# Optimization experiments

Hardware: AMD Instinct MI355X
Metric: run time of the kernel (lower is better)

Reference implementation:

```python
import jax, jax.numpy as jnp
import numpy as np

B, L, D, R, NTYPES, NLAYERS = 8, 96, 512, 64, 47, 3
BN_EPS = 1e-3  # keras BatchNormalization default epsilon


def setup_inputs() -> dict:
    key = jax.random.key(0)
    ks = jax.random.split(key, 12)
    text = jax.random.normal(ks[0], (B, L, D), dtype=jnp.float32)
    # binary token mask; force first token on so counts are never zero
    input_mask = (jax.random.uniform(ks[1], (B, L)) < 0.8).astype(jnp.float32)
    input_mask = input_mask.at[:, 0].set(1.0)
    dep_adj = (jax.random.uniform(ks[2], (B, L, L)) < 0.1).astype(jnp.float32)
    dep_value = jax.random.randint(ks[3], (B, L, L), 0, NTYPES, dtype=jnp.int32)
    dep_emb_table = jax.random.normal(ks[4], (NTYPES, D), dtype=jnp.float32) * 0.05
    bn_gamma = jnp.ones((D,), jnp.float32)
    bn_beta = jnp.zeros((D,), jnp.float32)
    W_stack = jax.random.normal(ks[5], (NLAYERS, D, D), dtype=jnp.float32) * 0.02
    b_stack = jax.random.normal(ks[6], (NLAYERS, D), dtype=jnp.float32) * 0.02
    ensemble_linear = jnp.ones((NLAYERS,), jnp.float32)
    fc_W = jax.random.normal(ks[7], (D, R), dtype=jnp.float32) * 0.02
    fc_b = jnp.zeros((R,), jnp.float32)
    return {"text": text, "input_mask": input_mask, "dep_adj": dep_adj,
            "dep_emb_table": dep_emb_table, "bn_gamma": bn_gamma, "bn_beta": bn_beta,
            "W_stack": W_stack, "b_stack": b_stack, "ensemble_linear": ensemble_linear,
            "fc_W": fc_W, "fc_b": fc_b, "dep_value": dep_value}


def _masked_avg(mask, x):
    # get_average: sum over masked tokens / count of nonzero mask entries
    m = mask[:, :, None]                       # [B,L,1]
    x_sum = jnp.sum(x * m, axis=1)             # [B,D]
    cnt = jnp.sum((m != 0).astype(x.dtype), axis=1)  # [B,1]
    return x_sum / (cnt + 1e-10)


def reference(text, input_mask, dep_adj, dep_emb_table, bn_gamma, bn_beta,
              W_stack, b_stack, ensemble_linear, fc_W, fc_b, dep_value):
    # dep embedding + switch_layer: zero out rows where dep type id == 0
    dep_embed = dep_emb_table[dep_value]                           # [B,L,L,D]
    dep_embed = dep_embed * (dep_value > 0)[..., None].astype(dep_embed.dtype)

    # BatchNormalization at inference (moving mean 0, var 1) + identity dropout
    seq = text * (bn_gamma / jnp.sqrt(1.0 + BN_EPS)) + bn_beta     # [B,L,D]

    scale = 1.0 / np.float32(np.power(D, 0.5))
    pools = []
    for l in range(NLAYERS):
        # get_attention: sum_k cat(x_i, e_ij)_k * cat(x_j, e_ji)_k
        #              = x_i . x_j + e_ij . e_ji
        score = (jnp.einsum('bid,bjd->bij', seq, seq)
                 + jnp.einsum('bijd,bjid->bij', dep_embed, dep_embed)) * scale
        attn = jax.nn.softmax(score, axis=-1) * dep_adj            # [B,L,L]
        # TypeGraphConvolution: out_i = sum_j attn_ij * ((x_j + e_ji) @ W) + b
        # (W applied after the attn-weighted aggregation; same linear math)
        agg = (jnp.einsum('bij,bjd->bid', attn, seq)
               + jnp.einsum('bij,bjid->bid', attn, dep_embed))      # [B,L,D]
        seq = jax.nn.relu(agg @ W_stack[l] + b_stack[l])
        pools.append(_masked_avg(input_mask, seq))

    x_pool = jnp.stack(pools, axis=-1)                              # [B,D,3]
    ens = jnp.sum(x_pool * jax.nn.softmax(ensemble_linear), axis=-1)  # [B,D]
    return ens @ fc_W + fc_b                                        # [B,R]
```

## Files before the change

### kernel.cpp

```cpp
#include <hip/hip_runtime.h>
#include <math.h>

#define SCALE 0.044194173824159216f
#define INVS  0.9995003746879289f

#define SEQ_OFF  0
#define AGG_OFF  393216
#define G_OFF    786432
#define POOL_OFF 788736
#define ENSW_OFF 801024
#define CNT_OFF  801028

#define F4FMA(acc, s, ww) { acc.x = fmaf(s, ww.x, acc.x); acc.y = fmaf(s, ww.y, acc.y); \
                            acc.z = fmaf(s, ww.z, acc.z); acc.w = fmaf(s, ww.w, acc.w); }

__device__ __forceinline__ float wave_sum(float v) {
  #pragma unroll
  for (int o = 32; o; o >>= 1) v += __shfl_xor(v, o);
  return v;
}
__device__ __forceinline__ float wave_max(float v) {
  #pragma unroll
  for (int o = 32; o; o >>= 1) v = fmaxf(v, __shfl_xor(v, o));
  return v;
}

__global__ __launch_bounds__(256) void k_prep(
    const float* __restrict__ text, const float* __restrict__ mask,
    const float* __restrict__ E, const float* __restrict__ gamma,
    const float* __restrict__ beta, const float* __restrict__ ensl,
    float* __restrict__ ws)
{
  const int blk = blockIdx.x, tid = threadIdx.x;
  const int gt = blk * 256 + tid;
  {
    const float4* T4 = (const float4*)text;
    float4* S4 = (float4*)(ws + SEQ_OFF);
    const float4* G4 = (const float4*)gamma;
    const float4* B4 = (const float4*)beta;
    for (int i4 = gt; i4 < 98304; i4 += 512 * 256) {
      float4 t = T4[i4];
      const int gi = i4 & 127;
      const float4 g4 = G4[gi], b4 = B4[gi];
      float4 o;
      o.x = fmaf(t.x, g4.x * INVS, b4.x);
      o.y = fmaf(t.y, g4.y * INVS, b4.y);
      o.z = fmaf(t.z, g4.z * INVS, b4.z);
      o.w = fmaf(t.w, g4.w * INVS, b4.w);
      S4[i4] = o;
    }
  }
  const int wg = gt >> 6, lane = tid & 63;
  float* G = ws + G_OFF;
  for (int g = wg; g < 2209; g += 2048) {
    const int t1 = g / 47, t2 = g - t1 * 47;
    const float4* e1 = (const float4*)E + t1 * 128;
    const float4* e2 = (const float4*)E + t2 * 128;
    const float4 a0 = e1[lane * 2], a1 = e1[lane * 2 + 1];
    const float4 b0 = e2[lane * 2], b1 = e2[lane * 2 + 1];
    float d = a0.x * b0.x;
    d = fmaf(a0.y, b0.y, d); d = fmaf(a0.z, b0.z, d); d = fmaf(a0.w, b0.w, d);
    d = fmaf(a1.x, b1.x, d); d = fmaf(a1.y, b1.y, d);
    d = fmaf(a1.z, b1.z, d); d = fmaf(a1.w, b1.w, d);
    d = wave_sum(d);
    if (lane == 0) G[g] = d;
  }
  if (blk == 0) {
    if (tid < 8) {
      float c = 0.f;
      for (int i = 0; i < 96; ++i) c += (mask[tid * 96 + i] != 0.f) ? 1.f : 0.f;
      (ws + CNT_OFF)[tid] = 1.f / (c + 1e-10f);
    }
    if (tid == 8) {
      const float e0 = ensl[0], e1 = ensl[1], e2 = ensl[2];
      const float m = fmaxf(e0, fmaxf(e1, e2));
      const float x0 = expf(e0 - m), x1 = expf(e1 - m), x2 = expf(e2 - m);
      const float s = x0 + x1 + x2;
      (ws + ENSW_OFF)[0] = x0 / s;
      (ws + ENSW_OFF)[1] = x1 / s;
      (ws + ENSW_OFF)[2] = x2 / s;
    }
  }
}

__device__ __forceinline__ void pool_unit(int u, int tid,
    const float* __restrict__ seq, const float* __restrict__ mask,
    const float* __restrict__ rcnt, float* __restrict__ dst)
{
  const int b = u >> 1;
  const int d = (u & 1) * 256 + tid;
  float acc = 0.f;
  #pragma unroll 4
  for (int i = 0; i < 96; ++i)
    acc = fmaf(mask[b * 96 + i], seq[(b * 96 + i) * 512 + d], acc);
  dst[b * 512 + d] = acc * rcnt[b];
}

__global__ __launch_bounds__(256) void k_attn(
    const float* __restrict__ seq, float* __restrict__ agg,
    const float* __restrict__ adj, const float* __restrict__ E,
    const int* __restrict__ dv, const float* __restrict__ ws,
    const float* __restrict__ mask, float* __restrict__ pool_dst, int do_pool)
{
  const int blk = blockIdx.x, tid = threadIdx.x;
  if (blk >= 768) {
    if (do_pool) pool_unit(blk - 768, tid, seq, mask, ws + CNT_OFF, pool_dst);
    return;
  }
  __shared__ float s_sc[96];
  __shared__ float s_at[96];
  __shared__ int   s_vt[96];
  const int b = blk & 7, i = blk >> 3;
  const int w = tid >> 6, lane = tid & 63;
  const float* G = ws + G_OFF;
  const float4* seq4 = (const float4*)seq + (size_t)b * 96 * 128;

  const float4 q0 = seq4[i * 128 + lane * 2];
  const float4 q1 = seq4[i * 128 + lane * 2 + 1];
  #pragma unroll 2
  for (int j = w; j < 96; j += 4) {
    const float4 x0 = seq4[j * 128 + lane * 2];
    const float4 x1 = seq4[j * 128 + lane * 2 + 1];
    float d = q0.x * x0.x;
    d = fmaf(q0.y, x0.y, d); d = fmaf(q0.z, x0.z, d); d = fmaf(q0.w, x0.w, d);
    d = fmaf(q1.x, x1.x, d); d = fmaf(q1.y, x1.y, d);
    d = fmaf(q1.z, x1.z, d); d = fmaf(q1.w, x1.w, d);
    d = wave_sum(d);
    if (lane == 0) s_sc[j] = d;
  }
  __syncthreads();
  const int* dvb = dv + b * 9216;
  if (tid < 96) {
    const int v1 = dvb[i * 96 + tid];
    const int v2 = dvb[tid * 96 + i];
    s_vt[tid] = v2;
    const float bs = (v1 > 0 && v2 > 0) ? G[v1 * 47 + v2] : 0.f;
    s_sc[tid] = (s_sc[tid] + bs) * SCALE;
  }
  __syncthreads();
  if (w == 0) {
    const float v0 = s_sc[lane];
    const float v1 = (lane < 32) ? s_sc[64 + lane] : -3.0e38f;
    const float mx = wave_max(fmaxf(v0, v1));
    const float e0 = expf(v0 - mx);
    const float e1 = (lane < 32) ? expf(v1 - mx) : 0.f;
    const float s = wave_sum(e0 + e1);
    const float inv = 1.f / s;
    const float* ad = adj + (b * 96 + i) * 96;
    s_at[lane] = e0 * inv * ad[lane];
    if (lane < 32) s_at[64 + lane] = e1 * inv * ad[64 + lane];
  }
  __syncthreads();
  const int d2 = w * 64 + lane;
  const float2* seq2 = (const float2*)seq + (size_t)b * 96 * 256;
  const float2* E2 = (const float2*)E;
  float ax = 0.f, ay = 0.f;
  for (int j = 0; j < 96; ++j) {
    const float a = s_at[j];
    if (a != 0.f) {
      float2 x = seq2[j * 256 + d2];
      const int vt = s_vt[j];
      if (vt > 0) {
        const float2 e2v = E2[vt * 256 + d2];
        x.x += e2v.x; x.y += e2v.y;
      }
      ax = fmaf(a, x.x, ax);
      ay = fmaf(a, x.y, ay);
    }
  }
  float2 o; o.x = ax; o.y = ay;
  ((float2*)agg)[(size_t)(b * 96 + i) * 256 + d2] = o;
}

__global__ __launch_bounds__(256) void k_gemm(
    const float* __restrict__ A, const float* __restrict__ W,
    const float* __restrict__ bias, float* __restrict__ Out)
{
  __shared__ __align__(16) float s_a[6 * 512];
  __shared__ __align__(16) float4 s_p[8 * 6 * 32];
  const int blk = blockIdx.x, tid = threadIdx.x;
  const int b = blk & 7, rr = (blk >> 3) & 15, ct = blk >> 7;
  const int rt = b * 16 + rr;
  const int r0 = rt * 6, c0 = ct * 128;
  {
    const float4* A4 = (const float4*)(A + r0 * 512);
    float4* sa4 = (float4*)s_a;
    sa4[tid] = A4[tid];
    sa4[tid + 256] = A4[tid + 256];
    sa4[tid + 512] = A4[tid + 512];
  }
  __syncthreads();
  const int cq = tid & 31, kq = tid >> 5;
  const float4* W4 = (const float4*)W + ct * 32 + cq;
  float4 acc[6];
  #pragma unroll
  for (int r = 0; r < 6; ++r) { acc[r].x = 0.f; acc[r].y = 0.f; acc[r].z = 0.f; acc[r].w = 0.f; }
  const float4* sa4 = (const float4*)s_a;
  #pragma unroll 2
  for (int k4 = kq * 16; k4 < kq * 16 + 16; ++k4) {
    const float4 w0 = W4[(k4 * 4 + 0) * 128];
    const float4 w1 = W4[(k4 * 4 + 1) * 128];
    const float4 w2 = W4[(k4 * 4 + 2) * 128];
    const float4 w3 = W4[(k4 * 4 + 3) * 128];
    #pragma unroll
    for (int r = 0; r < 6; ++r) {
      const float4 a4 = sa4[r * 128 + k4];
      F4FMA(acc[r], a4.x, w0); F4FMA(acc[r], a4.y, w1);
      F4FMA(acc[r], a4.z, w2); F4FMA(acc[r], a4.w, w3);
    }
  }
  #pragma unroll
  for (int r = 0; r < 6; ++r) s_p[(kq * 6 + r) * 32 + cq] = acc[r];
  __syncthreads();
  if (tid < 192) {
    const int r = tid >> 5, c = tid & 31;
    float4 s = s_p[r * 32 + c];
    #pragma unroll
    for (int q = 1; q < 8; ++q) {
      const float4 p = s_p[(q * 6 + r) * 32 + c];
      s.x += p.x; s.y += p.y; s.z += p.z; s.w += p.w;
    }
    const float4 bv = ((const float4*)(bias + c0))[c];
    float4 o;
    o.x = fmaxf(s.x + bv.x, 0.f);
    o.y = fmaxf(s.y + bv.y, 0.f);
    o.z = fmaxf(s.z + bv.z, 0.f);
    o.w = fmaxf(s.w + bv.w, 0.f);
    ((float4*)(Out + (size_t)(r0 + r) * 512 + c0))[c] = o;
  }
}

__global__ __launch_bounds__(256) void k_final(
    const float* __restrict__ seq, const float* __restrict__ mask,
    const float* __restrict__ ws, const float* __restrict__ fcW,
    const float* __restrict__ fcb, float* __restrict__ out)
{
  __shared__ float s_ens[512];
  __shared__ float s_red[256];
  const int b = blockIdx.x, tid = threadIdx.x;
  const float* ensw = ws + ENSW_OFF;
  const float* rcnt = ws + CNT_OFF;
  const float* p0 = ws + POOL_OFF + b * 512;
  const float* p1 = ws + POOL_OFF + 4096 + b * 512;
  float2 acc; acc.x = 0.f; acc.y = 0.f;
  const float2* seqb2 = (const float2*)(seq + (size_t)b * 96 * 512);
  #pragma unroll 4
  for (int i = 0; i < 96; ++i) {
    const float m = mask[b * 96 + i];
    const float2 x = seqb2[i * 256 + tid];
    acc.x = fmaf(m, x.x, acc.x);
    acc.y = fmaf(m, x.y, acc.y);
  }
  const float rc = rcnt[b];
  const float w0 = ensw[0], w1 = ensw[1], w2 = ensw[2];
  s_ens[tid * 2]     = w0 * p0[tid * 2]     + w1 * p1[tid * 2]     + w2 * acc.x * rc;
  s_ens[tid * 2 + 1] = w0 * p0[tid * 2 + 1] + w1 * p1[tid * 2 + 1] + w2 * acc.y * rc;
  __syncthreads();
  const int r = tid & 63, dq = tid >> 6;
  float a = 0.f;
  #pragma unroll 4
  for (int d = dq * 128; d < dq * 128 + 128; ++d)
    a = fmaf(s_ens[d], fcW[d * 64 + r], a);
  s_red[tid] = a;
  __syncthreads();
  if (tid < 64)
    out[b * 64 + tid] = fcb[tid] + s_red[tid] + s_red[64 + tid]
                      + s_red[128 + tid] + s_red[192 + tid];
}

extern "C" void kernel_launch(void* const* d_in, const int* in_sizes, int n_in,
                              void* d_out, int out_size, void* d_ws, size_t ws_size,
                              hipStream_t stream)
{
  const float* text  = (const float*)d_in[0];
  const float* mask  = (const float*)d_in[1];
  const float* adj   = (const float*)d_in[2];
  const float* E     = (const float*)d_in[3];
  const float* gamma = (const float*)d_in[4];
  const float* beta  = (const float*)d_in[5];
  const float* Wst   = (const float*)d_in[6];
  const float* bst   = (const float*)d_in[7];
  const float* ensl  = (const float*)d_in[8];
  const float* fcW   = (const float*)d_in[9];
  const float* fcb   = (const float*)d_in[10];
  const int*   dv    = (const int*)d_in[11];
  float* ws  = (float*)d_ws;
  float* out = (float*)d_out;

  float* seq = ws + SEQ_OFF;
  float* agg = ws + AGG_OFF;

  k_prep<<<dim3(512), dim3(256), 0, stream>>>(text, mask, E, gamma, beta, ensl, ws);
  for (int l = 0; l < 3; ++l) {
    k_attn<<<dim3(784), dim3(256), 0, stream>>>(
        seq, agg, adj, E, dv, ws, mask,
        ws + POOL_OFF + (l > 0 ? (l - 1) * 4096 : 0), l > 0 ? 1 : 0);
    k_gemm<<<dim3(512), dim3(256), 0, stream>>>(
        agg, Wst + l * 262144, bst + l * 512, seq);
  }
  k_final<<<dim3(8), dim3(256), 0, stream>>>(seq, mask, ws, fcW, fcb, out);
}
```

Before: 185.4 us.

## Process two query rows per attention block and split GEMM into narrower column tiles

The attention kernel now handles two query rows per block. Each key row it loads is reused for two dot products, the softmax is computed by two waves at once, and aggregation uses float4 loads, so the block count drops from 768 to 384. The GEMM moves from 128-column to 64-column tiles with a 16-way K split, which doubles the grid to 1024 blocks to raise parallelism, at the cost of re-reading the A tile from memory more often. Vector loads now use coalesced lane-contiguous float4 indexing rather than lane*2 strides.

```diff
diff --git a/kernel.cpp b/kernel.cpp
--- a/kernel.cpp
+++ b/kernel.cpp
@@ -56,8 +56,8 @@
     const int t1 = g / 47, t2 = g - t1 * 47;
     const float4* e1 = (const float4*)E + t1 * 128;
     const float4* e2 = (const float4*)E + t2 * 128;
-    const float4 a0 = e1[lane * 2], a1 = e1[lane * 2 + 1];
-    const float4 b0 = e2[lane * 2], b1 = e2[lane * 2 + 1];
+    const float4 a0 = e1[lane], a1 = e1[64 + lane];
+    const float4 b0 = e2[lane], b1 = e2[64 + lane];
     float d = a0.x * b0.x;
     d = fmaf(a0.y, b0.y, d); d = fmaf(a0.z, b0.z, d); d = fmaf(a0.w, b0.w, d);
     d = fmaf(a1.x, b1.x, d); d = fmaf(a1.y, b1.y, d);
@@ -103,73 +103,82 @@
     const float* __restrict__ mask, float* __restrict__ pool_dst, int do_pool)
 {
   const int blk = blockIdx.x, tid = threadIdx.x;
-  if (blk >= 768) {
-    if (do_pool) pool_unit(blk - 768, tid, seq, mask, ws + CNT_OFF, pool_dst);
+  if (blk >= 384) {
+    if (do_pool) pool_unit(blk - 384, tid, seq, mask, ws + CNT_OFF, pool_dst);
     return;
   }
-  __shared__ float s_sc[96];
-  __shared__ float s_at[96];
-  __shared__ int   s_vt[96];
-  const int b = blk & 7, i = blk >> 3;
+  __shared__ float s_sc[2][96];
+  __shared__ float s_at[2][96];
+  __shared__ int   s_vt[2][96];
+  const int b = blk & 7, ip = blk >> 3;
+  const int iA = ip * 2, iB = iA + 1;
   const int w = tid >> 6, lane = tid & 63;
   const float* G = ws + G_OFF;
   const float4* seq4 = (const float4*)seq + (size_t)b * 96 * 128;
 
-  const float4 q0 = seq4[i * 128 + lane * 2];
-  const float4 q1 = seq4[i * 128 + lane * 2 + 1];
+  const float4 qA0 = seq4[iA * 128 + lane];
+  const float4 qA1 = seq4[iA * 128 + 64 + lane];
+  const float4 qB0 = seq4[iB * 128 + lane];
+  const float4 qB1 = seq4[iB * 128 + 64 + lane];
   #pragma unroll 2
   for (int j = w; j < 96; j += 4) {
-    const float4 x0 = seq4[j * 128 + lane * 2];
-    const float4 x1 = seq4[j * 128 + lane * 2 + 1];
-    float d = q0.x * x0.x;
-    d = fmaf(q0.y, x0.y, d); d = fmaf(q0.z, x0.z, d); d = fmaf(q0.w, x0.w, d);
-    d = fmaf(q1.x, x1.x, d); d = fmaf(q1.y, x1.y, d);
-    d = fmaf(q1.z, x1.z, d); d = fmaf(q1.w, x1.w, d);
-    d = wave_sum(d);
-    if (lane == 0) s_sc[j] = d;
+    const float4 x0 = seq4[j * 128 + lane];
+    const float4 x1 = seq4[j * 128 + 64 + lane];
+    float dA = qA0.x * x0.x;
+    dA = fmaf(qA0.y, x0.y, dA); dA = fmaf(qA0.z, x0.z, dA); dA = fmaf(qA0.w, x0.w, dA);
+    dA = fmaf(qA1.x, x1.x, dA); dA = fmaf(qA1.y, x1.y, dA);
+    dA = fmaf(qA1.z, x1.z, dA); dA = fmaf(qA1.w, x1.w, dA);
+    float dB = qB0.x * x0.x;
+    dB = fmaf(qB0.y, x0.y, dB); dB = fmaf(qB0.z, x0.z, dB); dB = fmaf(qB0.w, x0.w, dB);
+    dB = fmaf(qB1.x, x1.x, dB); dB = fmaf(qB1.y, x1.y, dB);
+    dB = fmaf(qB1.z, x1.z, dB); dB = fmaf(qB1.w, x1.w, dB);
+    dA = wave_sum(dA);
+    dB = wave_sum(dB);
+    if (lane == 0) { s_sc[0][j] = dA; s_sc[1][j] = dB; }
   }
   __syncthreads();
   const int* dvb = dv + b * 9216;
-  if (tid < 96) {
-    const int v1 = dvb[i * 96 + tid];
-    const int v2 = dvb[tid * 96 + i];
-    s_vt[tid] = v2;
+  if (tid < 192) {
+    const int row = (tid >= 96) ? 1 : 0, jj = tid - row * 96;
+    const int i = iA + row;
+    const int v1 = dvb[i * 96 + jj];
+    const int v2 = dvb[jj * 96 + i];
+    s_vt[row][jj] = v2;
     const float bs = (v1 > 0 && v2 > 0) ? G[v1 * 47 + v2] : 0.f;
-    s_sc[tid] = (s_sc[tid] + bs) * SCALE;
-  }
-  __syncthreads();
-  if (w == 0) {
-    const float v0 = s_sc[lane];
-    const float v1 = (lane < 32) ? s_sc[64 + lane] : -3.0e38f;
+    s_sc[row][jj] = (s_sc[row][jj] + bs) * SCALE;
+  }
+  __syncthreads();
+  if (w < 2) {
+    const int i = iA + w;
+    const float v0 = s_sc[w][lane];
+    const float v1 = (lane < 32) ? s_sc[w][64 + lane] : -3.0e38f;
     const float mx = wave_max(fmaxf(v0, v1));
     const float e0 = expf(v0 - mx);
     const float e1 = (lane < 32) ? expf(v1 - mx) : 0.f;
     const float s = wave_sum(e0 + e1);
     const float inv = 1.f / s;
     const float* ad = adj + (b * 96 + i) * 96;
-    s_at[lane] = e0 * inv * ad[lane];
-    if (lane < 32) s_at[64 + lane] = e1 * inv * ad[64 + lane];
-  }
-  __syncthreads();
-  const int d2 = w * 64 + lane;
-  const float2* seq2 = (const float2*)seq + (size_t)b * 96 * 256;
-  const float2* E2 = (const float2*)E;
-  float ax = 0.f, ay = 0.f;
+    s_at[w][lane] = e0 * inv * ad[lane];
+    if (lane < 32) s_at[w][64 + lane] = e1 * inv * ad[64 + lane];
+  }
+  __syncthreads();
+  const int row = w & 1, i = iA + row;
+  const int d4 = (w >> 1) * 64 + lane;
+  const float4* E4 = (const float4*)E;
+  float4 ac = {0.f, 0.f, 0.f, 0.f};
   for (int j = 0; j < 96; ++j) {
-    const float a = s_at[j];
+    const float a = s_at[row][j];
     if (a != 0.f) {
-      float2 x = seq2[j * 256 + d2];
-      const int vt = s_vt[j];
+      float4 x = seq4[j * 128 + d4];
+      const int vt = s_vt[row][j];
       if (vt > 0) {
-        const float2 e2v = E2[vt * 256 + d2];
-        x.x += e2v.x; x.y += e2v.y;
+        const float4 e4 = E4[vt * 128 + d4];
+        x.x += e4.x; x.y += e4.y; x.z += e4.z; x.w += e4.w;
       }
-      ax = fmaf(a, x.x, ax);
-      ay = fmaf(a, x.y, ay);
-    }
-  }
-  float2 o; o.x = ax; o.y = ay;
-  ((float2*)agg)[(size_t)(b * 96 + i) * 256 + d2] = o;
+      F4FMA(ac, a, x);
+    }
+  }
+  ((float4*)agg)[(size_t)(b * 96 + i) * 128 + d4] = ac;
 }
 
 __global__ __launch_bounds__(256) void k_gemm(
@@ -177,11 +186,10 @@
     const float* __restrict__ bias, float* __restrict__ Out)
 {
   __shared__ __align__(16) float s_a[6 * 512];
-  __shared__ __align__(16) float4 s_p[8 * 6 * 32];
+  __shared__ __align__(16) float4 s_p[16 * 6 * 16];
   const int blk = blockIdx.x, tid = threadIdx.x;
   const int b = blk & 7, rr = (blk >> 3) & 15, ct = blk >> 7;
-  const int rt = b * 16 + rr;
-  const int r0 = rt * 6, c0 = ct * 128;
+  const int r0 = (b * 16 + rr) * 6, c0 = ct * 64;
   {
     const float4* A4 = (const float4*)(A + r0 * 512);
     float4* sa4 = (float4*)s_a;
@@ -190,14 +198,14 @@
     sa4[tid + 512] = A4[tid + 512];
   }
   __syncthreads();
-  const int cq = tid & 31, kq = tid >> 5;
-  const float4* W4 = (const float4*)W + ct * 32 + cq;
+  const int cq = tid & 15, kq = tid >> 4;
+  const float4* W4 = (const float4*)W + ct * 16 + cq;
   float4 acc[6];
   #pragma unroll
   for (int r = 0; r < 6; ++r) { acc[r].x = 0.f; acc[r].y = 0.f; acc[r].z = 0.f; acc[r].w = 0.f; }
   const float4* sa4 = (const float4*)s_a;
   #pragma unroll 2
-  for (int k4 = kq * 16; k4 < kq * 16 + 16; ++k4) {
+  for (int k4 = kq * 8; k4 < kq * 8 + 8; ++k4) {
     const float4 w0 = W4[(k4 * 4 + 0) * 128];
     const float4 w1 = W4[(k4 * 4 + 1) * 128];
     const float4 w2 = W4[(k4 * 4 + 2) * 128];
@@ -210,14 +218,14 @@
     }
   }
   #pragma unroll
-  for (int r = 0; r < 6; ++r) s_p[(kq * 6 + r) * 32 + cq] = acc[r];
-  __syncthreads();
-  if (tid < 192) {
-    const int r = tid >> 5, c = tid & 31;
-    float4 s = s_p[r * 32 + c];
+  for (int r = 0; r < 6; ++r) s_p[(kq * 6 + r) * 16 + cq] = acc[r];
+  __syncthreads();
+  if (tid < 96) {
+    const int r = tid >> 4, c = tid & 15;
+    float4 s = s_p[r * 16 + c];
     #pragma unroll
-    for (int q = 1; q < 8; ++q) {
-      const float4 p = s_p[(q * 6 + r) * 32 + c];
+    for (int q = 1; q < 16; ++q) {
+      const float4 p = s_p[(q * 6 + r) * 16 + c];
       s.x += p.x; s.y += p.y; s.z += p.z; s.w += p.w;
     }
     const float4 bv = ((const float4*)(bias + c0))[c];
@@ -292,10 +300,10 @@
 
   k_prep<<<dim3(512), dim3(256), 0, stream>>>(text, mask, E, gamma, beta, ensl, ws);
   for (int l = 0; l < 3; ++l) {
-    k_attn<<<dim3(784), dim3(256), 0, stream>>>(
+    k_attn<<<dim3(400), dim3(256), 0, stream>>>(
         seq, agg, adj, E, dv, ws, mask,
         ws + POOL_OFF + (l > 0 ? (l - 1) * 4096 : 0), l > 0 ? 1 : 0);
-    k_gemm<<<dim3(512), dim3(256), 0, stream>>>(
+    k_gemm<<<dim3(1024), dim3(256), 0, stream>>>(
         agg, Wst + l * 262144, bst + l * 512, seq);
   }
   k_final<<<dim3(8), dim3(256), 0, stream>>>(seq, mask, ws, fcW, fcb, out);
```

New measurement: 188.9 us. Within noise of the previous version (+1.9%).

## Compact nonzero attention entries, coalesce float4 loads, split GEMM into more column tiles

Applied to the files above, without the earlier changes.

In the attention kernel, the softmax wave now writes only the nonzero attention weights into a compacted list using a shared-memory atomic counter. The aggregation loop then walks that list instead of testing all 96 entries with divergent branches, and it adds the edge embedding through a select-multiply rather than a branch. The dot-product loads switch from interleaved lane*2 indexing to contiguous per-lane float4 indexing for better coalescing. The GEMM uses 64-column tiles with a 16-way k split, doubling the grid to 1024 blocks for more parallelism at the cost of a larger reduction and re-reading the A tile twice as often.

```diff
diff --git a/kernel.cpp b/kernel.cpp
--- a/kernel.cpp
+++ b/kernel.cpp
@@ -56,8 +56,8 @@
     const int t1 = g / 47, t2 = g - t1 * 47;
     const float4* e1 = (const float4*)E + t1 * 128;
     const float4* e2 = (const float4*)E + t2 * 128;
-    const float4 a0 = e1[lane * 2], a1 = e1[lane * 2 + 1];
-    const float4 b0 = e2[lane * 2], b1 = e2[lane * 2 + 1];
+    const float4 a0 = e1[lane], a1 = e1[64 + lane];
+    const float4 b0 = e2[lane], b1 = e2[64 + lane];
     float d = a0.x * b0.x;
     d = fmaf(a0.y, b0.y, d); d = fmaf(a0.z, b0.z, d); d = fmaf(a0.w, b0.w, d);
     d = fmaf(a1.x, b1.x, d); d = fmaf(a1.y, b1.y, d);
@@ -108,19 +108,23 @@
     return;
   }
   __shared__ float s_sc[96];
-  __shared__ float s_at[96];
   __shared__ int   s_vt[96];
+  __shared__ float s_ca[96];
+  __shared__ int   s_cj[96];
+  __shared__ int   s_cv[96];
+  __shared__ int   s_cnt;
   const int b = blk & 7, i = blk >> 3;
   const int w = tid >> 6, lane = tid & 63;
   const float* G = ws + G_OFF;
   const float4* seq4 = (const float4*)seq + (size_t)b * 96 * 128;
 
-  const float4 q0 = seq4[i * 128 + lane * 2];
-  const float4 q1 = seq4[i * 128 + lane * 2 + 1];
+  if (tid == 0) s_cnt = 0;
+  const float4 q0 = seq4[i * 128 + lane];
+  const float4 q1 = seq4[i * 128 + 64 + lane];
   #pragma unroll 2
   for (int j = w; j < 96; j += 4) {
-    const float4 x0 = seq4[j * 128 + lane * 2];
-    const float4 x1 = seq4[j * 128 + lane * 2 + 1];
+    const float4 x0 = seq4[j * 128 + lane];
+    const float4 x1 = seq4[j * 128 + 64 + lane];
     float d = q0.x * x0.x;
     d = fmaf(q0.y, x0.y, d); d = fmaf(q0.z, x0.z, d); d = fmaf(q0.w, x0.w, d);
     d = fmaf(q1.x, x1.x, d); d = fmaf(q1.y, x1.y, d);
@@ -147,29 +151,36 @@
     const float s = wave_sum(e0 + e1);
     const float inv = 1.f / s;
     const float* ad = adj + (b * 96 + i) * 96;
-    s_at[lane] = e0 * inv * ad[lane];
-    if (lane < 32) s_at[64 + lane] = e1 * inv * ad[64 + lane];
-  }
-  __syncthreads();
-  const int d2 = w * 64 + lane;
+    const float a0 = e0 * inv * ad[lane];
+    if (a0 != 0.f) {
+      const int p = atomicAdd(&s_cnt, 1);
+      s_cj[p] = lane; s_ca[p] = a0; s_cv[p] = s_vt[lane];
+    }
+    if (lane < 32) {
+      const float a1 = e1 * inv * ad[64 + lane];
+      if (a1 != 0.f) {
+        const int p = atomicAdd(&s_cnt, 1);
+        s_cj[p] = 64 + lane; s_ca[p] = a1; s_cv[p] = s_vt[64 + lane];
+      }
+    }
+  }
+  __syncthreads();
+  const int nnz = s_cnt;
   const float2* seq2 = (const float2*)seq + (size_t)b * 96 * 256;
-  const float2* E2 = (const float2*)E;
+  const float2* E2v = (const float2*)E;
   float ax = 0.f, ay = 0.f;
-  for (int j = 0; j < 96; ++j) {
-    const float a = s_at[j];
-    if (a != 0.f) {
-      float2 x = seq2[j * 256 + d2];
-      const int vt = s_vt[j];
-      if (vt > 0) {
-        const float2 e2v = E2[vt * 256 + d2];
-        x.x += e2v.x; x.y += e2v.y;
-      }
-      ax = fmaf(a, x.x, ax);
-      ay = fmaf(a, x.y, ay);
-    }
+  for (int t = 0; t < nnz; ++t) {
+    const float a = s_ca[t];
+    const int j = s_cj[t];
+    const int vt = s_cv[t];
+    const float2 x = seq2[j * 256 + tid];
+    const float2 ev = E2v[vt * 256 + tid];
+    const float sel = (vt > 0) ? 1.f : 0.f;
+    ax = fmaf(a, fmaf(sel, ev.x, x.x), ax);
+    ay = fmaf(a, fmaf(sel, ev.y, x.y), ay);
   }
   float2 o; o.x = ax; o.y = ay;
-  ((float2*)agg)[(size_t)(b * 96 + i) * 256 + d2] = o;
+  ((float2*)agg)[(size_t)(b * 96 + i) * 256 + tid] = o;
 }
 
 __global__ __launch_bounds__(256) void k_gemm(
@@ -177,11 +188,10 @@
     const float* __restrict__ bias, float* __restrict__ Out)
 {
   __shared__ __align__(16) float s_a[6 * 512];
-  __shared__ __align__(16) float4 s_p[8 * 6 * 32];
+  __shared__ __align__(16) float4 s_p[16 * 6 * 16];
   const int blk = blockIdx.x, tid = threadIdx.x;
   const int b = blk & 7, rr = (blk >> 3) & 15, ct = blk >> 7;
-  const int rt = b * 16 + rr;
-  const int r0 = rt * 6, c0 = ct * 128;
+  const int r0 = (b * 16 + rr) * 6, c0 = ct * 64;
   {
     const float4* A4 = (const float4*)(A + r0 * 512);
     float4* sa4 = (float4*)s_a;
@@ -190,14 +200,14 @@
     sa4[tid + 512] = A4[tid + 512];
   }
   __syncthreads();
-  const int cq = tid & 31, kq = tid >> 5;
-  const float4* W4 = (const float4*)W + ct * 32 + cq;
+  const int cq = tid & 15, kq = tid >> 4;
+  const float4* W4 = (const float4*)W + ct * 16 + cq;
   float4 acc[6];
   #pragma unroll
   for (int r = 0; r < 6; ++r) { acc[r].x = 0.f; acc[r].y = 0.f; acc[r].z = 0.f; acc[r].w = 0.f; }
   const float4* sa4 = (const float4*)s_a;
   #pragma unroll 2
-  for (int k4 = kq * 16; k4 < kq * 16 + 16; ++k4) {
+  for (int k4 = kq * 8; k4 < kq * 8 + 8; ++k4) {
     const float4 w0 = W4[(k4 * 4 + 0) * 128];
     const float4 w1 = W4[(k4 * 4 + 1) * 128];
     const float4 w2 = W4[(k4 * 4 + 2) * 128];
@@ -210,14 +220,14 @@
     }
   }
   #pragma unroll
-  for (int r = 0; r < 6; ++r) s_p[(kq * 6 + r) * 32 + cq] = acc[r];
-  __syncthreads();
-  if (tid < 192) {
-    const int r = tid >> 5, c = tid & 31;
-    float4 s = s_p[r * 32 + c];
+  for (int r = 0; r < 6; ++r) s_p[(kq * 6 + r) * 16 + cq] = acc[r];
+  __syncthreads();
+  if (tid < 96) {
+    const int r = tid >> 4, c = tid & 15;
+    float4 s = s_p[r * 16 + c];
     #pragma unroll
-    for (int q = 1; q < 8; ++q) {
-      const float4 p = s_p[(q * 6 + r) * 32 + c];
+    for (int q = 1; q < 16; ++q) {
+      const float4 p = s_p[(q * 6 + r) * 16 + c];
       s.x += p.x; s.y += p.y; s.z += p.z; s.w += p.w;
     }
     const float4 bv = ((const float4*)(bias + c0))[c];
@@ -295,7 +305,7 @@
     k_attn<<<dim3(784), dim3(256), 0, stream>>>(
         seq, agg, adj, E, dv, ws, mask,
         ws + POOL_OFF + (l > 0 ? (l - 1) * 4096 : 0), l > 0 ? 1 : 0);
-    k_gemm<<<dim3(512), dim3(256), 0, stream>>>(
+    k_gemm<<<dim3(1024), dim3(256), 0, stream>>>(
         agg, Wst + l * 262144, bst + l * 512, seq);
   }
   k_final<<<dim3(8), dim3(256), 0, stream>>>(seq, mask, ws, fcW, fcb, out);
```

After: 168.8 us. 8.9% less time.
